# Kernel tuning notes

Hardware: AMD Instinct MI355X
Metric: run time of the kernel (lower is better)

The kernel has to match this reference:

```python
import jax, jax.numpy as jnp
import numpy as np

VOCAB = 1500   # vocab_size
NE = 208       # n_embed
T = 256        # block_size
NH = 4         # n_head
HD = NE // NH  # head_size = 52
NL = 8         # n_layer
B = 256        # batch


def setup_inputs() -> dict:
    key = jax.random.key(0)
    ks = jax.random.split(key, 16)
    f = lambda k, shape: jax.random.normal(k, shape, jnp.float32) * 0.02
    return {
        "idx": jax.random.randint(ks[0], (B, T), 0, VOCAB),
        "targets": jax.random.randint(ks[1], (B, T), 0, VOCAB),
        "tok_emb": f(ks[2], (VOCAB, NE)),
        "pos_emb": f(ks[3], (T, NE)),
        # per-layer stacked attention params (separate no-bias Q/K/V Linears per head)
        "Wq": f(ks[4], (NL, NH, NE, HD)),
        "Wk": f(ks[5], (NL, NH, NE, HD)),
        "Wv": f(ks[6], (NL, NH, NE, HD)),
        "Wo": f(ks[7], (NL, NE, NE)),
        "bo": jnp.zeros((NL, NE), jnp.float32),
        "ln1_g": jnp.ones((NL, NE), jnp.float32),
        "ln1_b": jnp.zeros((NL, NE), jnp.float32),
        "W1": f(ks[8], (NL, NE, 4 * NE)),
        "b1": jnp.zeros((NL, 4 * NE), jnp.float32),
        "W2": f(ks[9], (NL, 4 * NE, NE)),
        "b2": jnp.zeros((NL, NE), jnp.float32),
        "ln2_g": jnp.ones((NL, NE), jnp.float32),
        "ln2_b": jnp.zeros((NL, NE), jnp.float32),
        "lnf_g": jnp.ones((NE,), jnp.float32),
        "lnf_b": jnp.zeros((NE,), jnp.float32),
        "Wlm": f(ks[10], (NE, VOCAB)),
        "blm": jnp.zeros((VOCAB,), jnp.float32),
    }


def _layernorm(x, g, b, eps=1e-5):
    mu = x.mean(-1, keepdims=True)
    var = ((x - mu) ** 2).mean(-1, keepdims=True)
    return (x - mu) * jax.lax.rsqrt(var + eps) * g + b


def reference(idx, targets, tok_emb, pos_emb, Wq, Wk, Wv, Wo, bo,
              ln1_g, ln1_b, W1, b1, W2, b2, ln2_g, ln2_b,
              lnf_g, lnf_b, Wlm, blm):
    x = tok_emb[idx] + pos_emb[None, :, :]          # [B, T, NE]
    mask = jnp.tril(jnp.ones((T, T), bool))
    scale = NE ** -0.5                               # NOTE: scales by n_embed, per source (C**-0.5)
    for i in range(NL):
        h = _layernorm(x, ln1_g[i], ln1_b[i])
        q = jnp.einsum('btc,hcd->bhtd', h, Wq[i])
        k = jnp.einsum('btc,hcd->bhtd', h, Wk[i])
        v = jnp.einsum('btc,hcd->bhtd', h, Wv[i])
        s = jnp.einsum('bhtd,bhsd->bhts', q, k) * scale
        s = jnp.where(mask, s, -jnp.inf)
        a = jax.nn.softmax(s, axis=-1)               # dropout is identity in eval
        o = jnp.einsum('bhts,bhsd->bhtd', a, v)
        o = o.transpose(0, 2, 1, 3).reshape(x.shape[0], T, NE)
        x = x + o @ Wo[i] + bo[i]
        h2 = _layernorm(x, ln2_g[i], ln2_b[i])
        x = x + jax.nn.relu(h2 @ W1[i] + b1[i]) @ W2[i] + b2[i]
    x = _layernorm(x, lnf_g, lnf_b)
    logits = (x @ Wlm + blm).reshape(-1, VOCAB)      # [B*T, VOCAB]
    logp = jax.nn.log_softmax(logits, axis=-1)
    loss = -jnp.take_along_axis(logp, targets.reshape(-1, 1), axis=-1).mean()
    return logits, loss
```

## Files before the change

kernel.cpp:

```cpp
#include <hip/hip_runtime.h>
#include <hip/hip_bf16.h>
#include <math.h>

#define VOCAB 1500
#define NE    208
#define TT    256
#define NHD   4
#define HD    52
#define NL    8
#define BBATCH 256
#define NTOK  (BBATCH * TT)
#define KP    224

typedef __attribute__((ext_vector_type(8))) short bf16x8;
typedef __attribute__((ext_vector_type(4))) short s16x4;
typedef __attribute__((ext_vector_type(4))) float f32x4;
typedef __attribute__((ext_vector_type(4))) int i32x4;
typedef __attribute__((ext_vector_type(4))) _Float16 f16x4;

__device__ __forceinline__ void gload16(const void* g, void* l) {
  __builtin_amdgcn_global_load_lds(
      (const __attribute__((address_space(1))) unsigned int*)g,
      (__attribute__((address_space(3))) unsigned int*)l, 16, 0, 0);
}
__device__ __forceinline__ float bf2f(short u) {
  union { unsigned int i; float f; } cv;
  cv.i = ((unsigned int)(unsigned short)u) << 16;
  return cv.f;
}
__device__ __forceinline__ short f2bf(float f) {
  return (short)__bfloat16_as_ushort(__float2bfloat16(f));
}

#define P_QKV 1146880
#define P_O   458752
#define P_1   1605632
#define P_2   1703936
#define P_LM  344064
__global__ __launch_bounds__(256) void k_prep_all(const float* __restrict__ Wq,
                                                  const float* __restrict__ Wk,
                                                  const float* __restrict__ Wv,
                                                  const float* __restrict__ Wo,
                                                  const float* __restrict__ W1,
                                                  const float* __restrict__ W2,
                                                  const float* __restrict__ Wlm,
                                                  __hip_bfloat16* __restrict__ qkvT,
                                                  __hip_bfloat16* __restrict__ oT,
                                                  __hip_bfloat16* __restrict__ t1,
                                                  __hip_bfloat16* __restrict__ t2,
                                                  __hip_bfloat16* __restrict__ lmT) {
  int gi = blockIdx.x * 256 + threadIdx.x;
  if (gi < P_QKV) {
    int i = gi;
    int c = i % KP;
    int jl = i / KP;
    int j = jl % 640, l = jl / 640;
    float v = 0.f;
    if (j < 624 && c < NE) {
      int sel = j / NE, hd = j - sel * NE;
      int h = hd / HD, d = hd - h * HD;
      const float* W = (sel == 0) ? Wq : (sel == 1) ? Wk : Wv;
      v = W[(((size_t)l * NHD + h) * NE + c) * HD + d];
    }
    qkvT[i] = __float2bfloat16(v);
  } else if (gi < P_QKV + P_O) {
    int i = gi - P_QKV;
    int c = i % KP;
    int jl = i / KP;
    int j = jl % 256, l = jl / 256;
    float v = (j < NE && c < NE) ? Wo[((size_t)l * NE + c) * NE + j] : 0.f;
    oT[i] = __float2bfloat16(v);
  } else if (gi < P_QKV + P_O + P_1) {
    int i = gi - (P_QKV + P_O);
    int c = i % KP;
    int jl = i / KP;
    int j = jl % 896, l = jl / 896;
    float v = (j < 832 && c < NE) ? W1[((size_t)l * NE + c) * 832 + j] : 0.f;
    t1[i] = __float2bfloat16(v);
  } else if (gi < P_QKV + P_O + P_1 + P_2) {
    int i = gi - (P_QKV + P_O + P_1);
    int c = i % 832;
    int jl = i / 832;
    int j = jl % 256, l = jl / 256;
    float v = (j < NE) ? W2[((size_t)l * 832 + c) * NE + j] : 0.f;
    t2[i] = __float2bfloat16(v);
  } else {
    int i = gi - (P_QKV + P_O + P_1 + P_2);
    int c = i % KP;
    int j = i / KP;
    float v = (j < VOCAB && c < NE) ? Wlm[(size_t)c * VOCAB + j] : 0.f;
    lmT[i] = __float2bfloat16(v);
  }
}

__global__ __launch_bounds__(256) void k_embed_ln(const int* __restrict__ idx,
                                                  const float* __restrict__ tok,
                                                  const float* __restrict__ pos,
                                                  const float* __restrict__ g,
                                                  const float* __restrict__ b,
                                                  __hip_bfloat16* __restrict__ x,
                                                  __hip_bfloat16* __restrict__ h) {
  int r = blockIdx.x * 4 + (threadIdx.x >> 6);
  int lane = threadIdx.x & 63;
  const int c0 = lane * 4;
  const int t = r & (TT - 1);
  float v[4] = {0.f, 0.f, 0.f, 0.f};
  float s = 0.f;
  if (lane < 52) {
    float4 tv = *(const float4*)(tok + (size_t)idx[r] * NE + c0);
    float4 pv = *(const float4*)(pos + (size_t)t * NE + c0);
    v[0] = tv.x + pv.x; v[1] = tv.y + pv.y;
    v[2] = tv.z + pv.z; v[3] = tv.w + pv.w;
    s = v[0] + v[1] + v[2] + v[3];
  }
  #pragma unroll
  for (int o = 32; o; o >>= 1) s += __shfl_xor(s, o);
  float mu = s * (1.f / NE);
  float q = 0.f;
  if (lane < 52) {
    #pragma unroll
    for (int i = 0; i < 4; i++) { float d = v[i] - mu; q += d * d; }
  }
  #pragma unroll
  for (int o = 32; o; o >>= 1) q += __shfl_xor(q, o);
  float inv = rsqrtf(q * (1.f / NE) + 1e-5f);
  if (lane < 52) {
    s16x4 xv;
    #pragma unroll
    for (int i = 0; i < 4; i++) xv[i] = f2bf(v[i]);
    *(s16x4*)(x + (size_t)r * NE + c0) = xv;
  }
  if (lane < 56) {
    s16x4 outv = {};
    if (lane < 52) {
      #pragma unroll
      for (int i = 0; i < 4; i++)
        outv[i] = f2bf((v[i] - mu) * inv * g[c0 + i] + b[c0 + i]);
    }
    *(s16x4*)(h + (size_t)r * KP + c0) = outv;
  }
}

template <bool RELU, bool BIAS, bool OUTBF, bool EXPSUM>
__global__ __launch_bounds__(256) void k_mgemm(const __hip_bfloat16* __restrict__ A, int lda,
                                               const __hip_bfloat16* __restrict__ BT, int ldb,
                                               const float* __restrict__ bias,
                                               void* __restrict__ Cout, int ldc,
                                               int N, int K,
                                               float* __restrict__ esum) {
  __shared__ __hip_bfloat16 As[2][128 * 32];
  __shared__ __hip_bfloat16 Bs[2][128 * 32];
  const int gx = gridDim.x;
  const int id = blockIdx.x + gx * blockIdx.y;
  const int qq = (gx * gridDim.y) >> 3;
  const int wid2 = (id & 7) * qq + (id >> 3);
  const int by = wid2 / gx, bx = wid2 - by * gx;
  const int bm = by * 128, bn = bx * 128;
  const int tid = threadIdx.x;
  const int wave = tid >> 6, lane = tid & 63;
  const int wr = (wave >> 1) * 64, wc = (wave & 1) * 64;
  const int l15 = lane & 15, l4 = lane >> 4;
  const int srow = tid >> 2, sgrp = (tid & 3) * 8;
  const int srow2 = srow + 64;
  f32x4 acc[4][4] = {};
  const int nt = K / 32;
  gload16(A + (size_t)(bm + srow) * lda + sgrp, &As[0][tid * 8]);
  gload16(BT + (size_t)(bn + srow) * ldb + sgrp, &Bs[0][tid * 8]);
  gload16(A + (size_t)(bm + srow2) * lda + sgrp, &As[0][(256 + tid) * 8]);
  gload16(BT + (size_t)(bn + srow2) * ldb + sgrp, &Bs[0][(256 + tid) * 8]);
  int cur = 0;
  for (int t = 0; t < nt; t++) {
    if (t + 1 < nt) {
      int k1 = (t + 1) * 32;
      gload16(A + (size_t)(bm + srow) * lda + k1 + sgrp, &As[cur ^ 1][tid * 8]);
      gload16(BT + (size_t)(bn + srow) * ldb + k1 + sgrp, &Bs[cur ^ 1][tid * 8]);
      gload16(A + (size_t)(bm + srow2) * lda + k1 + sgrp, &As[cur ^ 1][(256 + tid) * 8]);
      gload16(BT + (size_t)(bn + srow2) * ldb + k1 + sgrp, &Bs[cur ^ 1][(256 + tid) * 8]);
      asm volatile("s_waitcnt vmcnt(4)" ::: "memory");
    } else {
      asm volatile("s_waitcnt vmcnt(0)" ::: "memory");
    }
    __builtin_amdgcn_s_barrier();
    bf16x8 af[4], bfr[4];
    #pragma unroll
    for (int m = 0; m < 4; m++)
      af[m] = *(const bf16x8*)&As[cur][(wr + m * 16 + l15) * 32 + l4 * 8];
    #pragma unroll
    for (int n = 0; n < 4; n++)
      bfr[n] = *(const bf16x8*)&Bs[cur][(wc + n * 16 + l15) * 32 + l4 * 8];
    #pragma unroll
    for (int m = 0; m < 4; m++)
      #pragma unroll
      for (int n = 0; n < 4; n++)
        acc[m][n] = __builtin_amdgcn_mfma_f32_16x16x32_bf16(af[m], bfr[n], acc[m][n], 0, 0, 0);
    if (t + 1 < nt) __builtin_amdgcn_s_barrier();
    cur ^= 1;
  }
  float es[4][4];
  if (EXPSUM) {
    #pragma unroll
    for (int m = 0; m < 4; m++)
      #pragma unroll
      for (int j = 0; j < 4; j++) es[m][j] = 0.f;
  }
  #pragma unroll
  for (int m = 0; m < 4; m++) {
    #pragma unroll
    for (int n = 0; n < 4; n++) {
      int col = bn + wc + n * 16 + l15;
      if (col < N) {
        float bv = BIAS ? bias[col] : 0.f;
        #pragma unroll
        for (int j = 0; j < 4; j++) {
          int row = bm + wr + m * 16 + l4 * 4 + j;
          float v = acc[m][n][j] + bv;
          if (RELU) v = fmaxf(v, 0.f);
          size_t off = (size_t)row * ldc + col;
          if (OUTBF) ((__hip_bfloat16*)Cout)[off] = __float2bfloat16(v);
          else       ((float*)Cout)[off] = v;
          if (EXPSUM) es[m][j] += __expf(v);
        }
      }
    }
  }
  if (EXPSUM) {
    #pragma unroll
    for (int m = 0; m < 4; m++)
      #pragma unroll
      for (int j = 0; j < 4; j++) {
        float e = es[m][j];
        #pragma unroll
        for (int off = 1; off < 16; off <<= 1) e += __shfl_xor(e, off);
        if (l15 == 0) {
          int row = bm + wr + m * 16 + l4 * 4 + j;
          esum[(size_t)row * 24 + bx * 2 + (wave & 1)] = e;
        }
      }
  }
}

__global__ __launch_bounds__(512) void k_mgemm_ln(const __hip_bfloat16* __restrict__ A, int lda,
                                                  const __hip_bfloat16* __restrict__ BT, int ldb,
                                                  const float* __restrict__ bias,
                                                  const __hip_bfloat16* __restrict__ resid,
                                                  const float* __restrict__ g,
                                                  const float* __restrict__ bb,
                                                  __hip_bfloat16* __restrict__ xout,
                                                  __hip_bfloat16* __restrict__ hout,
                                                  int K) {
  __shared__ __hip_bfloat16 As[2][128 * 32];
  __shared__ __hip_bfloat16 Bs[2][256 * 32];
  __shared__ float red[128][4];
  const int bm = blockIdx.x * 128;
  const int tid = threadIdx.x;
  const int wid = tid >> 6, lane = tid & 63;
  const int wr = (wid >> 1) * 32, wc = (wid & 1) * 128;
  const int l15 = lane & 15, l4 = lane >> 4;
  const int srow = tid >> 2, sgrp = (tid & 3) * 8;
  f32x4 acc[2][8] = {};
  const int nt = K / 32;
  gload16(A + (size_t)(bm + srow) * lda + sgrp, &As[0][tid * 8]);
  gload16(BT + (size_t)srow * ldb + sgrp, &Bs[0][tid * 8]);
  gload16(BT + (size_t)(128 + srow) * ldb + sgrp, &Bs[0][(512 + tid) * 8]);
  int cur = 0;
  for (int t = 0; t < nt; t++) {
    if (t + 1 < nt) {
      int k1 = (t + 1) * 32;
      gload16(A + (size_t)(bm + srow) * lda + k1 + sgrp, &As[cur ^ 1][tid * 8]);
      gload16(BT + (size_t)srow * ldb + k1 + sgrp, &Bs[cur ^ 1][tid * 8]);
      gload16(BT + (size_t)(128 + srow) * ldb + k1 + sgrp, &Bs[cur ^ 1][(512 + tid) * 8]);
      asm volatile("s_waitcnt vmcnt(3)" ::: "memory");
    } else {
      asm volatile("s_waitcnt vmcnt(0)" ::: "memory");
    }
    __builtin_amdgcn_s_barrier();
    bf16x8 af[2], bfr[8];
    #pragma unroll
    for (int m = 0; m < 2; m++)
      af[m] = *(const bf16x8*)&As[cur][(wr + m * 16 + l15) * 32 + l4 * 8];
    #pragma unroll
    for (int n = 0; n < 8; n++)
      bfr[n] = *(const bf16x8*)&Bs[cur][(wc + n * 16 + l15) * 32 + l4 * 8];
    #pragma unroll
    for (int m = 0; m < 2; m++)
      #pragma unroll
      for (int n = 0; n < 8; n++)
        acc[m][n] = __builtin_amdgcn_mfma_f32_16x16x32_bf16(af[m], bfr[n], acc[m][n], 0, 0, 0);
    if (t + 1 < nt) __builtin_amdgcn_s_barrier();
    cur ^= 1;
  }
  #pragma unroll
  for (int m = 0; m < 2; m++)
    #pragma unroll
    for (int n = 0; n < 8; n++) {
      int col = wc + n * 16 + l15;
      #pragma unroll
      for (int j = 0; j < 4; j++) {
        int row = bm + wr + m * 16 + l4 * 4 + j;
        float v = 0.f;
        if (col < NE)
          v = acc[m][n][j] + bias[col] + __bfloat162float(resid[(size_t)row * NE + col]);
        acc[m][n][j] = v;
      }
    }
  #pragma unroll
  for (int m = 0; m < 2; m++)
    #pragma unroll
    for (int j = 0; j < 4; j++) {
      float s = 0.f, q = 0.f;
      #pragma unroll
      for (int n = 0; n < 8; n++) { float v = acc[m][n][j]; s += v; q += v * v; }
      #pragma unroll
      for (int off = 1; off < 16; off <<= 1) {
        s += __shfl_xor(s, off);
        q += __shfl_xor(q, off);
      }
      if (l15 == 0) {
        int row = wr + m * 16 + l4 * 4 + j;
        red[row][(wid & 1) * 2 + 0] = s;
        red[row][(wid & 1) * 2 + 1] = q;
      }
    }
  __syncthreads();
  #pragma unroll
  for (int m = 0; m < 2; m++)
    #pragma unroll
    for (int j = 0; j < 4; j++) {
      int lrow = wr + m * 16 + l4 * 4 + j;
      float s = red[lrow][0] + red[lrow][2];
      float q = red[lrow][1] + red[lrow][3];
      float mu = s * (1.f / NE);
      float var = q * (1.f / NE) - mu * mu;
      float inv = rsqrtf(var + 1e-5f);
      size_t row = bm + lrow;
      #pragma unroll
      for (int n = 0; n < 8; n++) {
        int col = wc + n * 16 + l15;
        if (col < NE) {
          float v = acc[m][n][j];
          xout[row * NE + col] = __float2bfloat16(v);
          hout[row * KP + col] = __float2bfloat16((v - mu) * inv * g[col] + bb[col]);
        } else if (col < KP) {
          hout[row * KP + col] = __float2bfloat16(0.f);
        }
      }
    }
}

__global__ __launch_bounds__(512) void k_mlp_ln(const __hip_bfloat16* __restrict__ h,
                                                const __hip_bfloat16* __restrict__ W1T,
                                                const float* __restrict__ b1,
                                                const __hip_bfloat16* __restrict__ W2T,
                                                const float* __restrict__ b2,
                                                const float* __restrict__ g,
                                                const float* __restrict__ bb,
                                                __hip_bfloat16* __restrict__ xio,
                                                __hip_bfloat16* __restrict__ hout) {
  __shared__ __hip_bfloat16 Hs[128 * 232];
  __shared__ __hip_bfloat16 W1s[64 * 224];
  __shared__ __hip_bfloat16 Ac[128 * 72];
  __shared__ __hip_bfloat16 W2s[2][256 * 32];
  __shared__ float sred[128][4], qred[128][4];
  const int bm = blockIdx.x * 128;
  const int tid = threadIdx.x;
  const int wid = tid >> 6, lane = tid & 63;
  const int l15 = lane & 15, l4 = lane >> 4;
  const int w1r = (wid >> 1) * 32, w1c = (wid & 1) * 32;
  const int w2r = (wid >> 2) * 64, w2c = (wid & 3) * 64;
  #pragma unroll
  for (int it = 0; it < 14; it++) {
    int slot = it * 512 + tid;
    int row = slot / 56, gq = slot - row * 56;
    *(s16x4*)&Hs[row * 232 + gq * 4] =
        *(const s16x4*)(h + (size_t)(bm + row) * KP + gq * 4);
  }
  f32x4 acc2[4][4] = {};
  for (int jc = 0; jc < 13; jc++) {
    if (jc) __syncthreads();
    for (int s = tid; s < 1792; s += 512)
      gload16(W1T + (size_t)(jc * 64 + s / 28) * KP + (s % 28) * 8, &W1s[s * 8]);
    for (int s = tid; s < 2048; s += 512) {
      int kt2 = s >> 10, ss = s & 1023;
      gload16(W2T + (size_t)(ss >> 2) * 832 + jc * 64 + kt2 * 32 + (ss & 3) * 8,
              &W2s[kt2][ss * 8]);
    }
    __syncthreads();
    f32x4 acc1[2][2] = {};
    #pragma unroll
    for (int kt = 0; kt < 7; kt++) {
      bf16x8 a0 = *(const bf16x8*)&Hs[(w1r + l15) * 232 + kt * 32 + l4 * 8];
      bf16x8 a1 = *(const bf16x8*)&Hs[(w1r + 16 + l15) * 232 + kt * 32 + l4 * 8];
      bf16x8 c0 = *(const bf16x8*)&W1s[(w1c + l15) * 224 + kt * 32 + l4 * 8];
      bf16x8 c1 = *(const bf16x8*)&W1s[(w1c + 16 + l15) * 224 + kt * 32 + l4 * 8];
      acc1[0][0] = __builtin_amdgcn_mfma_f32_16x16x32_bf16(a0, c0, acc1[0][0], 0, 0, 0);
      acc1[0][1] = __builtin_amdgcn_mfma_f32_16x16x32_bf16(a0, c1, acc1[0][1], 0, 0, 0);
      acc1[1][0] = __builtin_amdgcn_mfma_f32_16x16x32_bf16(a1, c0, acc1[1][0], 0, 0, 0);
      acc1[1][1] = __builtin_amdgcn_mfma_f32_16x16x32_bf16(a1, c1, acc1[1][1], 0, 0, 0);
    }
    #pragma unroll
    for (int m = 0; m < 2; m++)
      #pragma unroll
      for (int n = 0; n < 2; n++) {
        int colL = w1c + n * 16 + l15;
        float bv = b1[jc * 64 + colL];
        #pragma unroll
        for (int j = 0; j < 4; j++) {
          int rowL = w1r + m * 16 + l4 * 4 + j;
          Ac[rowL * 72 + colL] = __float2bfloat16(fmaxf(acc1[m][n][j] + bv, 0.f));
        }
      }
    __syncthreads();
    #pragma unroll
    for (int kt2 = 0; kt2 < 2; kt2++) {
      bf16x8 af[4], bfr[4];
      #pragma unroll
      for (int m = 0; m < 4; m++)
        af[m] = *(const bf16x8*)&Ac[(w2r + m * 16 + l15) * 72 + kt2 * 32 + l4 * 8];
      #pragma unroll
      for (int n = 0; n < 4; n++)
        bfr[n] = *(const bf16x8*)&W2s[kt2][(w2c + n * 16 + l15) * 32 + l4 * 8];
      #pragma unroll
      for (int m = 0; m < 4; m++)
        #pragma unroll
        for (int n = 0; n < 4; n++)
          acc2[m][n] = __builtin_amdgcn_mfma_f32_16x16x32_bf16(af[m], bfr[n], acc2[m][n], 0, 0, 0);
    }
  }
  #pragma unroll
  for (int m2 = 0; m2 < 4; m2++)
    #pragma unroll
    for (int j = 0; j < 4; j++) {
      int rowL = w2r + m2 * 16 + l4 * 4 + j;
      float s = 0.f, q = 0.f;
      #pragma unroll
      for (int n2 = 0; n2 < 4; n2++) {
        int col = w2c + n2 * 16 + l15;
        float v = 0.f;
        if (col < NE)
          v = acc2[m2][n2][j] + b2[col] +
              __bfloat162float(xio[(size_t)(bm + rowL) * NE + col]);
        acc2[m2][n2][j] = v;
        s += v; q += v * v;
      }
      #pragma unroll
      for (int off = 1; off < 16; off <<= 1) {
        s += __shfl_xor(s, off);
        q += __shfl_xor(q, off);
      }
      if (l15 == 0) { sred[rowL][wid & 3] = s; qred[rowL][wid & 3] = q; }
    }
  __syncthreads();
  #pragma unroll
  for (int m2 = 0; m2 < 4; m2++)
    #pragma unroll
    for (int j = 0; j < 4; j++) {
      int rowL = w2r + m2 * 16 + l4 * 4 + j;
      float s = sred[rowL][0] + sred[rowL][1] + sred[rowL][2] + sred[rowL][3];
      float q = qred[rowL][0] + qred[rowL][1] + qred[rowL][2] + qred[rowL][3];
      float mu = s * (1.f / NE);
      float var = q * (1.f / NE) - mu * mu;
      float inv = rsqrtf(var + 1e-5f);
      size_t row = bm + rowL;
      #pragma unroll
      for (int n2 = 0; n2 < 4; n2++) {
        int col = w2c + n2 * 16 + l15;
        if (col < NE) {
          float v = acc2[m2][n2][j];
          xio[row * NE + col] = __float2bfloat16(v);
          hout[row * KP + col] = __float2bfloat16((v - mu) * inv * g[col] + bb[col]);
        } else if (col < KP) {
          hout[row * KP + col] = __float2bfloat16(0.f);
        }
      }
    }
}

#define KSTRIDE 64
#define VSTRIDE 260
__global__ __launch_bounds__(256) void k_attn_mfma(const __hip_bfloat16* __restrict__ qkv,
                                                   __hip_bfloat16* __restrict__ o) {
  __shared__ __hip_bfloat16 Ks[256 * KSTRIDE];
  __shared__ _Float16      Vt[64 * VSTRIDE];
  const int bh0 = blockIdx.x;
  const int bh = (bh0 & 7) * 128 + (bh0 >> 3);
  const int b = bh >> 2, h = bh & 3;
  const __hip_bfloat16* base = qkv + (size_t)b * TT * 624;
  const int tid = threadIdx.x;
  #pragma unroll
  for (int it = 0; it < 16; it++) {
    int u = it * 256 + tid;
    int t = u >> 4, d4 = (u & 15) * 4;
    s16x4 v = {};
    if (d4 < 52) v = *(const s16x4*)(base + t * 624 + 208 + h * HD + d4);
    *(s16x4*)&Ks[t * KSTRIDE + d4] = v;
  }
  #pragma unroll
  for (int it = 0; it < 13; it++) {
    int slot = it * 256 + tid;
    int t = slot / 13, dl = (slot - t * 13) * 4;
    s16x4 kv = *(const s16x4*)(base + t * 624 + 416 + h * HD + dl);
    #pragma unroll
    for (int i = 0; i < 4; i++)
      Vt[(dl + i) * VSTRIDE + t] = (_Float16)bf2f(kv[i]);
  }
  #pragma unroll
  for (int it = 0; it < 12; it++)
    Vt[(52 + it) * VSTRIDE + tid] = (_Float16)0.f;
  __syncthreads();

  const int w = tid >> 6, lane = tid & 63, l15 = lane & 15, l4 = lane >> 4;
  const float scale = 0.06933752453f;
  const int qts[4] = {w, 7 - w, 8 + w, 15 - w};
  bf16x8 qf[4][2];
  #pragma unroll
  for (int i = 0; i < 4; i++) {
    const __hip_bfloat16* qrow = base + (qts[i] * 16 + l15) * 624 + h * HD;
    #pragma unroll
    for (int ks = 0; ks < 2; ks++) {
      int s = ks * 32 + l4 * 8;
      union { s16x4 h2[2]; bf16x8 v; } u;
      u.h2[0] = (s <= 48) ? *(const s16x4*)(qrow + s) : (s16x4){};
      u.h2[1] = (s <= 44) ? *(const s16x4*)(qrow + s + 4) : (s16x4){};
      qf[i][ks] = u.v;
    }
  }
  f32x4 oacc[4][4] = {};
  float mrun[4] = {-1e30f, -1e30f, -1e30f, -1e30f};
  float lrun[4] = {0.f, 0.f, 0.f, 0.f};
  const int cmax = 15 - w;
  for (int c = 0; c <= cmax; c++) {
    const int kb = c * 16;
    const bf16x8 kf0 = *(const bf16x8*)&Ks[(kb + l15) * KSTRIDE + l4 * 8];
    const bf16x8 kf1 = *(const bf16x8*)&Ks[(kb + l15) * KSTRIDE + 32 + l4 * 8];
    #pragma unroll
    for (int i = 0; i < 4; i++) {
      if (qts[i] < c) continue;
      __builtin_amdgcn_s_setprio(1);
      f32x4 s4 = __builtin_amdgcn_mfma_f32_16x16x32_bf16(kf0, qf[i][0],
                                                         (f32x4){0.f, 0.f, 0.f, 0.f}, 0, 0, 0);
      s4 = __builtin_amdgcn_mfma_f32_16x16x32_bf16(kf1, qf[i][1], s4, 0, 0, 0);
      __builtin_amdgcn_s_setprio(0);
      const int q = qts[i] * 16 + l15;
      float pv[4];
      float pmax = -1e30f;
      #pragma unroll
      for (int j = 0; j < 4; j++) {
        int key = kb + l4 * 4 + j;
        float s = s4[j] * scale;
        pv[j] = (key <= q) ? s : -1e30f;
        pmax = fmaxf(pmax, pv[j]);
      }
      pmax = fmaxf(pmax, __shfl_xor(pmax, 16));
      pmax = fmaxf(pmax, __shfl_xor(pmax, 32));
      if (!__all(pmax - mrun[i] <= 8.f)) {
        const float newm = fmaxf(mrun[i], pmax);
        const float r = __expf(mrun[i] - newm);
        lrun[i] *= r;
        mrun[i] = newm;
        #pragma unroll
        for (int m = 0; m < 4; m++) {
          oacc[m][i][0] *= r; oacc[m][i][1] *= r;
          oacc[m][i][2] *= r; oacc[m][i][3] *= r;
        }
      }
      float psum = 0.f;
      f16x4 pb;
      #pragma unroll
      for (int j = 0; j < 4; j++) {
        float e = __expf(pv[j] - mrun[i]);
        psum += e;
        pb[j] = (_Float16)e;
      }
      psum += __shfl_xor(psum, 16);
      psum += __shfl_xor(psum, 32);
      lrun[i] += psum;
      __builtin_amdgcn_s_setprio(1);
      #pragma unroll
      for (int m = 0; m < 4; m++) {
        f16x4 vf = *(const f16x4*)&Vt[(m * 16 + l15) * VSTRIDE + kb + l4 * 4];
        oacc[m][i] = __builtin_amdgcn_mfma_f32_16x16x16f16(vf, pb, oacc[m][i], 0, 0, 0);
      }
      __builtin_amdgcn_s_setprio(0);
    }
  }
  #pragma unroll
  for (int i = 0; i < 4; i++) {
    const float inv = 1.f / lrun[i];
    __hip_bfloat16* orow = o + (size_t)(b * TT + qts[i] * 16 + l15) * KP + h * HD;
    #pragma unroll
    for (int m = 0; m < 4; m++) {
      int d0 = m * 16 + l4 * 4;
      if (d0 + 3 < HD) {
        s16x4 pk;
        #pragma unroll
        for (int j = 0; j < 4; j++) pk[j] = f2bf(oacc[m][i][j] * inv);
        *(s16x4*)(orow + d0) = pk;
      }
    }
  }
}

__global__ __launch_bounds__(256) void k_loss_fin(const float* __restrict__ esum,
                                                  const float* __restrict__ logits,
                                                  const int* __restrict__ targets,
                                                  float* __restrict__ row_loss) {
  int r = blockIdx.x * 256 + threadIdx.x;
  const float* e = esum + (size_t)r * 24;
  float s = 0.f;
  #pragma unroll
  for (int i = 0; i < 24; i++) s += e[i];
  row_loss[r] = __logf(s) - logits[(size_t)r * VOCAB + targets[r]];
}

__global__ __launch_bounds__(256) void k_loss_reduce(const float* __restrict__ row_loss,
                                                     float* __restrict__ out_loss) {
  __shared__ float sh[256];
  float s = 0.f;
  for (int i = threadIdx.x; i < NTOK; i += 256) s += row_loss[i];
  sh[threadIdx.x] = s;
  __syncthreads();
  for (int k = 128; k; k >>= 1) {
    if (threadIdx.x < k) sh[threadIdx.x] += sh[threadIdx.x + k];
    __syncthreads();
  }
  if (threadIdx.x == 0) *out_loss = sh[0] * (1.f / NTOK);
}

extern "C" void kernel_launch(void* const* d_in, const int* in_sizes, int n_in,
                              void* d_out, int out_size, void* d_ws, size_t ws_size,
                              hipStream_t stream) {
  const int*   idx     = (const int*)d_in[0];
  const int*   targets = (const int*)d_in[1];
  const float* tok     = (const float*)d_in[2];
  const float* pos     = (const float*)d_in[3];
  const float* Wq      = (const float*)d_in[4];
  const float* Wk      = (const float*)d_in[5];
  const float* Wv      = (const float*)d_in[6];
  const float* Wo      = (const float*)d_in[7];
  const float* bo      = (const float*)d_in[8];
  const float* ln1g    = (const float*)d_in[9];
  const float* ln1b    = (const float*)d_in[10];
  const float* W1      = (const float*)d_in[11];
  const float* b1      = (const float*)d_in[12];
  const float* W2      = (const float*)d_in[13];
  const float* b2      = (const float*)d_in[14];
  const float* ln2g    = (const float*)d_in[15];
  const float* ln2b    = (const float*)d_in[16];
  const float* lnfg    = (const float*)d_in[17];
  const float* lnfb    = (const float*)d_in[18];
  const float* Wlm     = (const float*)d_in[19];
  const float* blm     = (const float*)d_in[20];
  float* out = (float*)d_out;

  char* w = (char*)d_ws;
  __hip_bfloat16* x   = (__hip_bfloat16*)w; w += (size_t)NTOK * NE * 2;
  __hip_bfloat16* qkv = (__hip_bfloat16*)w; w += (size_t)NTOK * 624 * 2;
  __hip_bfloat16* hbf = (__hip_bfloat16*)w; w += (size_t)NTOK * KP * 2;
  __hip_bfloat16* WqkvT = (__hip_bfloat16*)w; w += (size_t)P_QKV * 2;
  __hip_bfloat16* WoT   = (__hip_bfloat16*)w; w += (size_t)P_O * 2;
  __hip_bfloat16* W1T   = (__hip_bfloat16*)w; w += (size_t)P_1 * 2;
  __hip_bfloat16* W2T   = (__hip_bfloat16*)w; w += (size_t)P_2 * 2;
  __hip_bfloat16* WlmT  = (__hip_bfloat16*)w; w += (size_t)P_LM * 2;
  float* row_loss = (float*)w;              w += (size_t)NTOK * 4;
  float* esum     = (float*)w;

  k_prep_all<<<(P_QKV + P_O + P_1 + P_2 + P_LM) / 256, 256, 0, stream>>>(
      Wq, Wk, Wv, Wo, W1, W2, Wlm, WqkvT, WoT, W1T, W2T, WlmT);
  k_embed_ln<<<NTOK / 4, 256, 0, stream>>>(idx, tok, pos, ln1g, ln1b, x, hbf);

  for (int l = 0; l < NL; l++) {
    k_mgemm<false, false, true, false><<<dim3(5, 512), 256, 0, stream>>>(
        hbf, KP, WqkvT + (size_t)l * 640 * KP, KP, nullptr, qkv, 624, 624, KP, nullptr);
    k_attn_mfma<<<BBATCH * NHD, 256, 0, stream>>>(qkv, hbf);
    k_mgemm_ln<<<512, 512, 0, stream>>>(
        hbf, KP, WoT + (size_t)l * 256 * KP, KP, bo + l * NE, x,
        ln2g + l * NE, ln2b + l * NE, x, hbf, KP);
    const float* gn = (l < NL - 1) ? (ln1g + (l + 1) * NE) : lnfg;
    const float* bn = (l < NL - 1) ? (ln1b + (l + 1) * NE) : lnfb;
    k_mlp_ln<<<512, 512, 0, stream>>>(
        hbf, W1T + (size_t)l * 896 * KP, b1 + l * 832,
        W2T + (size_t)l * 256 * 832, b2 + l * NE, gn, bn, x, hbf);
  }

  k_mgemm<false, true, false, true><<<dim3(12, 512), 256, 0, stream>>>(
      hbf, KP, WlmT, KP, blm, out, VOCAB, VOCAB, KP, esum);

  k_loss_fin<<<NTOK / 256, 256, 0, stream>>>(esum, out, targets, row_loss);
  k_loss_reduce<<<1, 256, 0, stream>>>(row_loss, out + ((size_t)out_size - 1));
}
```

Baseline: 2.351 ms.

## Fuse Wo projection with LN2 and MLP into one kernel

Merges the attention output projection plus residual plus LayerNorm kernel into the MLP kernel. The LN2 output is written straight into shared memory instead of round-tripping through global memory, and the post-attention residual stays in registers for the MLP residual add. Shared memory is pooled so the Wo-stage tiles and the MLP-stage tiles reuse the same space. This removes one launch per layer and the global write and read of the intermediate h and x, at the cost of more registers and a longer serial kernel per block.

```diff
diff --git a/kernel.cpp b/kernel.cpp
--- a/kernel.cpp
+++ b/kernel.cpp
@@ -239,141 +239,114 @@
   }
 }
 
-__global__ __launch_bounds__(512) void k_mgemm_ln(const __hip_bfloat16* __restrict__ A, int lda,
-                                                  const __hip_bfloat16* __restrict__ BT, int ldb,
-                                                  const float* __restrict__ bias,
-                                                  const __hip_bfloat16* __restrict__ resid,
-                                                  const float* __restrict__ g,
-                                                  const float* __restrict__ bb,
-                                                  __hip_bfloat16* __restrict__ xout,
-                                                  __hip_bfloat16* __restrict__ hout,
-                                                  int K) {
-  __shared__ __hip_bfloat16 As[2][128 * 32];
-  __shared__ __hip_bfloat16 Bs[2][256 * 32];
-  __shared__ float red[128][4];
-  const int bm = blockIdx.x * 128;
-  const int tid = threadIdx.x;
-  const int wid = tid >> 6, lane = tid & 63;
-  const int wr = (wid >> 1) * 32, wc = (wid & 1) * 128;
-  const int l15 = lane & 15, l4 = lane >> 4;
-  const int srow = tid >> 2, sgrp = (tid & 3) * 8;
-  f32x4 acc[2][8] = {};
-  const int nt = K / 32;
-  gload16(A + (size_t)(bm + srow) * lda + sgrp, &As[0][tid * 8]);
-  gload16(BT + (size_t)srow * ldb + sgrp, &Bs[0][tid * 8]);
-  gload16(BT + (size_t)(128 + srow) * ldb + sgrp, &Bs[0][(512 + tid) * 8]);
-  int cur = 0;
-  for (int t = 0; t < nt; t++) {
-    if (t + 1 < nt) {
-      int k1 = (t + 1) * 32;
-      gload16(A + (size_t)(bm + srow) * lda + k1 + sgrp, &As[cur ^ 1][tid * 8]);
-      gload16(BT + (size_t)srow * ldb + k1 + sgrp, &Bs[cur ^ 1][tid * 8]);
-      gload16(BT + (size_t)(128 + srow) * ldb + k1 + sgrp, &Bs[cur ^ 1][(512 + tid) * 8]);
-      asm volatile("s_waitcnt vmcnt(3)" ::: "memory");
-    } else {
-      asm volatile("s_waitcnt vmcnt(0)" ::: "memory");
-    }
-    __builtin_amdgcn_s_barrier();
-    bf16x8 af[2], bfr[8];
-    #pragma unroll
-    for (int m = 0; m < 2; m++)
-      af[m] = *(const bf16x8*)&As[cur][(wr + m * 16 + l15) * 32 + l4 * 8];
-    #pragma unroll
-    for (int n = 0; n < 8; n++)
-      bfr[n] = *(const bf16x8*)&Bs[cur][(wc + n * 16 + l15) * 32 + l4 * 8];
-    #pragma unroll
-    for (int m = 0; m < 2; m++)
-      #pragma unroll
-      for (int n = 0; n < 8; n++)
-        acc[m][n] = __builtin_amdgcn_mfma_f32_16x16x32_bf16(af[m], bfr[n], acc[m][n], 0, 0, 0);
-    if (t + 1 < nt) __builtin_amdgcn_s_barrier();
-    cur ^= 1;
-  }
-  #pragma unroll
-  for (int m = 0; m < 2; m++)
-    #pragma unroll
-    for (int n = 0; n < 8; n++) {
-      int col = wc + n * 16 + l15;
-      #pragma unroll
-      for (int j = 0; j < 4; j++) {
-        int row = bm + wr + m * 16 + l4 * 4 + j;
-        float v = 0.f;
-        if (col < NE)
-          v = acc[m][n][j] + bias[col] + __bfloat162float(resid[(size_t)row * NE + col]);
-        acc[m][n][j] = v;
-      }
-    }
-  #pragma unroll
-  for (int m = 0; m < 2; m++)
-    #pragma unroll
-    for (int j = 0; j < 4; j++) {
-      float s = 0.f, q = 0.f;
-      #pragma unroll
-      for (int n = 0; n < 8; n++) { float v = acc[m][n][j]; s += v; q += v * v; }
-      #pragma unroll
-      for (int off = 1; off < 16; off <<= 1) {
-        s += __shfl_xor(s, off);
-        q += __shfl_xor(q, off);
-      }
-      if (l15 == 0) {
-        int row = wr + m * 16 + l4 * 4 + j;
-        red[row][(wid & 1) * 2 + 0] = s;
-        red[row][(wid & 1) * 2 + 1] = q;
-      }
-    }
-  __syncthreads();
-  #pragma unroll
-  for (int m = 0; m < 2; m++)
-    #pragma unroll
-    for (int j = 0; j < 4; j++) {
-      int lrow = wr + m * 16 + l4 * 4 + j;
-      float s = red[lrow][0] + red[lrow][2];
-      float q = red[lrow][1] + red[lrow][3];
-      float mu = s * (1.f / NE);
-      float var = q * (1.f / NE) - mu * mu;
-      float inv = rsqrtf(var + 1e-5f);
-      size_t row = bm + lrow;
-      #pragma unroll
-      for (int n = 0; n < 8; n++) {
-        int col = wc + n * 16 + l15;
-        if (col < NE) {
-          float v = acc[m][n][j];
-          xout[row * NE + col] = __float2bfloat16(v);
-          hout[row * KP + col] = __float2bfloat16((v - mu) * inv * g[col] + bb[col]);
-        } else if (col < KP) {
-          hout[row * KP + col] = __float2bfloat16(0.f);
-        }
-      }
-    }
-}
-
-__global__ __launch_bounds__(512) void k_mlp_ln(const __hip_bfloat16* __restrict__ h,
-                                                const __hip_bfloat16* __restrict__ W1T,
-                                                const float* __restrict__ b1,
-                                                const __hip_bfloat16* __restrict__ W2T,
-                                                const float* __restrict__ b2,
-                                                const float* __restrict__ g,
-                                                const float* __restrict__ bb,
-                                                __hip_bfloat16* __restrict__ xio,
-                                                __hip_bfloat16* __restrict__ hout) {
+__global__ __launch_bounds__(512) void k_wo_mlp_ln(const __hip_bfloat16* __restrict__ hattn,
+                                                   const __hip_bfloat16* __restrict__ WoT,
+                                                   const float* __restrict__ bo,
+                                                   const __hip_bfloat16* __restrict__ W1T,
+                                                   const float* __restrict__ b1,
+                                                   const __hip_bfloat16* __restrict__ W2T,
+                                                   const float* __restrict__ b2,
+                                                   const float* __restrict__ g2,
+                                                   const float* __restrict__ bb2,
+                                                   const float* __restrict__ gn,
+                                                   const float* __restrict__ bn,
+                                                   __hip_bfloat16* __restrict__ xio,
+                                                   __hip_bfloat16* __restrict__ hout) {
   __shared__ __hip_bfloat16 Hs[128 * 232];
-  __shared__ __hip_bfloat16 W1s[64 * 224];
-  __shared__ __hip_bfloat16 Ac[128 * 72];
-  __shared__ __hip_bfloat16 W2s[2][256 * 32];
+  __shared__ __hip_bfloat16 pool[39936];
+  __hip_bfloat16 (*As)[128 * 32] = (__hip_bfloat16 (*)[128 * 32])pool;
+  __hip_bfloat16 (*Bs)[256 * 32] = (__hip_bfloat16 (*)[256 * 32])(pool + 8192);
+  __hip_bfloat16* W1s = pool;
+  __hip_bfloat16* Ac  = pool + 14336;
+  __hip_bfloat16 (*W2s)[256 * 32] = (__hip_bfloat16 (*)[256 * 32])(pool + 23552);
   __shared__ float sred[128][4], qred[128][4];
   const int bm = blockIdx.x * 128;
   const int tid = threadIdx.x;
   const int wid = tid >> 6, lane = tid & 63;
   const int l15 = lane & 15, l4 = lane >> 4;
+  const int w2r = (wid >> 2) * 64, w2c = (wid & 3) * 64;
   const int w1r = (wid >> 1) * 32, w1c = (wid & 1) * 32;
-  const int w2r = (wid >> 2) * 64, w2c = (wid & 3) * 64;
-  #pragma unroll
-  for (int it = 0; it < 14; it++) {
-    int slot = it * 512 + tid;
-    int row = slot / 56, gq = slot - row * 56;
-    *(s16x4*)&Hs[row * 232 + gq * 4] =
-        *(const s16x4*)(h + (size_t)(bm + row) * KP + gq * 4);
-  }
+  const int srow = tid >> 2, sgrp = (tid & 3) * 8;
+  f32x4 xp[4][4] = {};
+  {
+    gload16(hattn + (size_t)(bm + srow) * KP + sgrp, &As[0][tid * 8]);
+    gload16(WoT + (size_t)srow * KP + sgrp, &Bs[0][tid * 8]);
+    gload16(WoT + (size_t)(128 + srow) * KP + sgrp, &Bs[0][(512 + tid) * 8]);
+    int cur = 0;
+    for (int t = 0; t < 7; t++) {
+      if (t + 1 < 7) {
+        int k1 = (t + 1) * 32;
+        gload16(hattn + (size_t)(bm + srow) * KP + k1 + sgrp, &As[cur ^ 1][tid * 8]);
+        gload16(WoT + (size_t)srow * KP + k1 + sgrp, &Bs[cur ^ 1][tid * 8]);
+        gload16(WoT + (size_t)(128 + srow) * KP + k1 + sgrp, &Bs[cur ^ 1][(512 + tid) * 8]);
+        asm volatile("s_waitcnt vmcnt(3)" ::: "memory");
+      } else {
+        asm volatile("s_waitcnt vmcnt(0)" ::: "memory");
+      }
+      __builtin_amdgcn_s_barrier();
+      bf16x8 af[4], bfr[4];
+      #pragma unroll
+      for (int m = 0; m < 4; m++)
+        af[m] = *(const bf16x8*)&As[cur][(w2r + m * 16 + l15) * 32 + l4 * 8];
+      #pragma unroll
+      for (int n = 0; n < 4; n++)
+        bfr[n] = *(const bf16x8*)&Bs[cur][(w2c + n * 16 + l15) * 32 + l4 * 8];
+      #pragma unroll
+      for (int m = 0; m < 4; m++)
+        #pragma unroll
+        for (int n = 0; n < 4; n++)
+          xp[m][n] = __builtin_amdgcn_mfma_f32_16x16x32_bf16(af[m], bfr[n], xp[m][n], 0, 0, 0);
+      if (t + 1 < 7) __builtin_amdgcn_s_barrier();
+      cur ^= 1;
+    }
+  }
+  #pragma unroll
+  for (int m = 0; m < 4; m++)
+    #pragma unroll
+    for (int j = 0; j < 4; j++) {
+      int rowL = w2r + m * 16 + l4 * 4 + j;
+      float s = 0.f, q = 0.f;
+      #pragma unroll
+      for (int n = 0; n < 4; n++) {
+        int col = w2c + n * 16 + l15;
+        float v = 0.f;
+        if (col < NE)
+          v = xp[m][n][j] + bo[col] +
+              bf2f(((const short*)xio)[(size_t)(bm + rowL) * NE + col]);
+        xp[m][n][j] = v;
+        s += v; q += v * v;
+      }
+      #pragma unroll
+      for (int off = 1; off < 16; off <<= 1) {
+        s += __shfl_xor(s, off);
+        q += __shfl_xor(q, off);
+      }
+      if (l15 == 0) { sred[rowL][wid & 3] = s; qred[rowL][wid & 3] = q; }
+    }
+  __syncthreads();
+  #pragma unroll
+  for (int m = 0; m < 4; m++)
+    #pragma unroll
+    for (int j = 0; j < 4; j++) {
+      int rowL = w2r + m * 16 + l4 * 4 + j;
+      float s = sred[rowL][0] + sred[rowL][1] + sred[rowL][2] + sred[rowL][3];
+      float q = qred[rowL][0] + qred[rowL][1] + qred[rowL][2] + qred[rowL][3];
+      float mu = s * (1.f / NE);
+      float var = q * (1.f / NE) - mu * mu;
+      float inv = rsqrtf(var + 1e-5f);
+      #pragma unroll
+      for (int n = 0; n < 4; n++) {
+        int col = w2c + n * 16 + l15;
+        if (col < NE)
+          Hs[rowL * 232 + col] =
+              __float2bfloat16((xp[m][n][j] - mu) * inv * g2[col] + bb2[col]);
+      }
+    }
+  {
+    int row = tid >> 2, c0 = 208 + (tid & 3) * 4;
+    *(s16x4*)&Hs[row * 232 + c0] = (s16x4){};
+  }
+  __syncthreads();
   f32x4 acc2[4][4] = {};
   for (int jc = 0; jc < 13; jc++) {
     if (jc) __syncthreads();
@@ -436,9 +409,7 @@
       for (int n2 = 0; n2 < 4; n2++) {
         int col = w2c + n2 * 16 + l15;
         float v = 0.f;
-        if (col < NE)
-          v = acc2[m2][n2][j] + b2[col] +
-              __bfloat162float(xio[(size_t)(bm + rowL) * NE + col]);
+        if (col < NE) v = acc2[m2][n2][j] + b2[col] + xp[m2][n2][j];
         acc2[m2][n2][j] = v;
         s += v; q += v * v;
       }
@@ -467,7 +438,7 @@
         if (col < NE) {
           float v = acc2[m2][n2][j];
           xio[row * NE + col] = __float2bfloat16(v);
-          hout[row * KP + col] = __float2bfloat16((v - mu) * inv * g[col] + bb[col]);
+          hout[row * KP + col] = __float2bfloat16((v - mu) * inv * gn[col] + bn[col]);
         } else if (col < KP) {
           hout[row * KP + col] = __float2bfloat16(0.f);
         }
@@ -672,14 +643,13 @@
     k_mgemm<false, false, true, false><<<dim3(5, 512), 256, 0, stream>>>(
         hbf, KP, WqkvT + (size_t)l * 640 * KP, KP, nullptr, qkv, 624, 624, KP, nullptr);
     k_attn_mfma<<<BBATCH * NHD, 256, 0, stream>>>(qkv, hbf);
-    k_mgemm_ln<<<512, 512, 0, stream>>>(
-        hbf, KP, WoT + (size_t)l * 256 * KP, KP, bo + l * NE, x,
-        ln2g + l * NE, ln2b + l * NE, x, hbf, KP);
-    const float* gn = (l < NL - 1) ? (ln1g + (l + 1) * NE) : lnfg;
-    const float* bn = (l < NL - 1) ? (ln1b + (l + 1) * NE) : lnfb;
-    k_mlp_ln<<<512, 512, 0, stream>>>(
-        hbf, W1T + (size_t)l * 896 * KP, b1 + l * 832,
-        W2T + (size_t)l * 256 * 832, b2 + l * NE, gn, bn, x, hbf);
+    const float* gnp = (l < NL - 1) ? (ln1g + (l + 1) * NE) : lnfg;
+    const float* bnp = (l < NL - 1) ? (ln1b + (l + 1) * NE) : lnfb;
+    k_wo_mlp_ln<<<512, 512, 0, stream>>>(
+        hbf, WoT + (size_t)l * 256 * KP, bo + l * NE,
+        W1T + (size_t)l * 896 * KP, b1 + l * 832,
+        W2T + (size_t)l * 256 * 832, b2 + l * NE,
+        ln2g + l * NE, ln2b + l * NE, gnp, bnp, x, hbf);
   }
 
   k_mgemm<false, true, false, true><<<dim3(12, 512), 256, 0, stream>>>(
```

Result: faster. 2.296 ms (-2.4%).
